# Kernel tuning notes

Hardware: AMD Instinct MI355X
Metric: run time of the kernel (lower is better)

Reference implementation:

```python
import jax, jax.numpy as jnp
import numpy as np

K = 31  # AvgPool2d kernel size
P = 15  # padding


def _box_avg(x):
    """31x31 stride-1 avg pool, count_include_pad=True (PyTorch default):
    separable ones-conv with zero padding, divided by K*K."""
    B, C, H, W = x.shape
    kh = jnp.ones((C, 1, K, 1), x.dtype)
    kw = jnp.ones((C, 1, 1, K), x.dtype)
    dn = ('NCHW', 'OIHW', 'NCHW')
    y = jax.lax.conv_general_dilated(x, kh, (1, 1), [(P, P), (0, 0)],
                                     dimension_numbers=dn, feature_group_count=C)
    y = jax.lax.conv_general_dilated(y, kw, (1, 1), [(0, 0), (P, P)],
                                     dimension_numbers=dn, feature_group_count=C)
    return y / (K * K)


def setup_inputs() -> dict:
    key = jax.random.key(0)
    k1, k2 = jax.random.split(key)
    pred = jax.random.normal(k1, (64, 1, 512, 512), dtype=jnp.float32)
    mask = jax.random.uniform(k2, (64, 1, 512, 512), dtype=jnp.float32)
    return {"pred": pred, "mask": mask}


def reference(pred, mask):
    weit = 1.0 + 5.0 * jnp.abs(_box_avg(mask) - mask)
    p = jax.nn.sigmoid(pred)
    inter = jnp.sum(p * mask * weit, axis=(2, 3))          # [B, C]
    union = jnp.sum((p + mask) * weit, axis=(2, 3))        # [B, C]
    wdiss = 1.0 - (2.0 * inter + 0.5) / (union + 0.5)
    return jnp.mean(wdiss)
```

## Files before the change

### kernel.cpp

```cpp
#include <hip/hip_runtime.h>
#include <math.h>

#define NB 64
#define HH 512
#define WW 512
#define KK 31
#define PP 15
#define TSP 128
#define NSP (HH / TSP)
#define RING 64
#define RMASK (RING - 1)

typedef _Float16 f16;
typedef f16 f16x8 __attribute__((ext_vector_type(8)));
typedef f16 f16x4 __attribute__((ext_vector_type(4)));
typedef f16 f16x2 __attribute__((ext_vector_type(2)));

__device__ __forceinline__ f16x2 shfl_up2(f16x2 v, int delta) {
    int x = __shfl_up(__builtin_bit_cast(int, v), delta);
    return __builtin_bit_cast(f16x2, x);
}
__device__ __forceinline__ f16x2 shfl_dn2(f16x2 v, int delta) {
    int x = __shfl_down(__builtin_bit_cast(int, v), delta);
    return __builtin_bit_cast(f16x2, x);
}
__device__ __forceinline__ f16x2 sel2(bool c, f16x2 v) {
    f16x2 z = {(f16)0, (f16)0};
    return c ? v : z;
}
__device__ __forceinline__ void memfence_sched() { asm volatile("" ::: "memory"); }

__device__ __forceinline__ void load_pair(
        const float* __restrict__ mb, const int y0, const int p,
        const int xbase, float (&va)[8], float (&vb)[8])
{
    const int gy0 = y0 + 2 * p - PP;
    const int gy1 = gy0 + 1;
    if (gy0 >= 0 && gy0 < HH) {
        const float* row = mb + (size_t)gy0 * WW + xbase;
        const float4 u = *(const float4*)(row);
        const float4 v = *(const float4*)(row + 4);
        va[0] = u.x; va[1] = u.y; va[2] = u.z; va[3] = u.w;
        va[4] = v.x; va[5] = v.y; va[6] = v.z; va[7] = v.w;
    } else {
        #pragma unroll
        for (int j = 0; j < 8; ++j) va[j] = 0.0f;
    }
    if (gy1 >= 0 && gy1 < HH) {
        const float* row = mb + (size_t)gy1 * WW + xbase;
        const float4 u = *(const float4*)(row);
        const float4 v = *(const float4*)(row + 4);
        vb[0] = u.x; vb[1] = u.y; vb[2] = u.z; vb[3] = u.w;
        vb[4] = v.x; vb[5] = v.y; vb[6] = v.z; vb[7] = v.w;
    } else {
        #pragma unroll
        for (int j = 0; j < 8; ++j) vb[j] = 0.0f;
    }
}

__device__ __forceinline__ void compute_pair(
        f16 (* __restrict__ Hs)[WW], f16 (* __restrict__ Ms)[WW],
        const int p, const int xbase, const int lane,
        const float (&va)[8], const float (&vb)[8])
{
    const bool lm1 = (lane >= 1);
    const bool lm2 = (lane >= 2);
    const bool lp1 = (lane <= 62);
    const bool lp2 = (lane <= 61);
    const int h0 = 2 * p;

    const int yr0 = h0 - PP;
    if (yr0 >= 0 && yr0 < TSP) {
        f16x8 mv;
        #pragma unroll
        for (int j = 0; j < 8; ++j) mv[j] = (f16)va[j];
        *(f16x8*)&Ms[yr0 & RMASK][xbase] = mv;
    }
    if (yr0 + 1 >= 0 && yr0 + 1 < TSP) {
        f16x8 mv;
        #pragma unroll
        for (int j = 0; j < 8; ++j) mv[j] = (f16)vb[j];
        *(f16x8*)&Ms[(yr0 + 1) & RMASK][xbase] = mv;
    }

    float sa[8], sb[8];
    sa[0] = va[0]; sb[0] = vb[0];
    #pragma unroll
    for (int j = 1; j < 8; ++j) { sa[j] = sa[j-1] + va[j]; sb[j] = sb[j-1] + vb[j]; }

    f16x2 ps[8];
    #pragma unroll
    for (int j = 0; j < 8; ++j)
        ps[j] = __builtin_bit_cast(f16x2, __builtin_amdgcn_cvt_pkrtz(sa[j], sb[j]));
    const f16x2 pT = ps[7];

    f16x2 A[7];
    #pragma unroll
    for (int j = 0; j < 7; ++j) A[j] = shfl_up2(pT - ps[j], 2);
    const f16x2 Bprev = shfl_up2(pT, 1);
    const f16x2 Cfull = shfl_dn2(pT, 1);
    f16x2 Cp[7];
    #pragma unroll
    for (int j = 0; j < 7; ++j) Cp[j] = shfl_dn2(ps[j], 2);

    f16x2 base = pT;
    base += sel2(lm1, Bprev);
    base += sel2(lp1, Cfull);

    f16x8 ha, hb;
    #pragma unroll
    for (int j = 0; j < 8; ++j) {
        f16x2 acc = base;
        if (j < 7) acc += sel2(lm2, A[j]);
        if (j > 0) acc += sel2(lp2, Cp[j-1]);
        ha[j] = acc[0];
        hb[j] = acc[1];
    }
    *(f16x8*)&Hs[h0 & RMASK][xbase] = ha;
    *(f16x8*)&Hs[(h0 + 1) & RMASK][xbase] = hb;
}

__device__ __forceinline__ void phase2_half(
        const float* __restrict__ pb,
        const f16 (* __restrict__ Hs)[WW], const f16 (* __restrict__ Ms)[WW],
        const int y0, const int r0h, const int c,
        float4& I4, float4& U4)
{
    float4 Pq[8];
    #pragma unroll
    for (int i = 0; i < 8; ++i)
        Pq[i] = *(const float4*)(pb + (size_t)(y0 + r0h + i) * WW + c);
    memfence_sched();

    f16x4 hl8[8], he8[8];
    f16x4 accA = {(f16)0, (f16)0, (f16)0, (f16)0};
    f16x4 accB = {(f16)0, (f16)0, (f16)0, (f16)0};
    #pragma unroll
    for (int j = 0; j < 8; ++j) {
        hl8[j] = *(const f16x4*)&Hs[(r0h + j) & RMASK][c];
        accA += hl8[j];
    }
    #pragma unroll
    for (int j = 8; j < 15; ++j) accA += *(const f16x4*)&Hs[(r0h + j) & RMASK][c];
    #pragma unroll
    for (int j = 15; j < 30; ++j) accB += *(const f16x4*)&Hs[(r0h + j) & RMASK][c];
    #pragma unroll
    for (int i = 0; i < 8; ++i) he8[i] = *(const f16x4*)&Hs[(r0h + 30 + i) & RMASK][c];

    float4 B;
    B.x = (float)accA[0] + (float)accB[0];
    B.y = (float)accA[1] + (float)accB[1];
    B.z = (float)accA[2] + (float)accB[2];
    B.w = (float)accA[3] + (float)accB[3];

    const float inv2 = 1.0f / (float)(KK * KK);

    #pragma unroll
    for (int i = 0; i < 8; ++i) {
        const int yr = r0h + i;
        const f16x4 he = he8[i];
        const f16x4 hl = hl8[i];
        const f16x4 mm = *(const f16x4*)&Ms[yr & RMASK][c];
        const float4 p4 = Pq[i];
        const float m0 = (float)mm[0], m1 = (float)mm[1];
        const float m2 = (float)mm[2], m3 = (float)mm[3];

        B.x += (float)he[0]; B.y += (float)he[1]; B.z += (float)he[2]; B.w += (float)he[3];

        const float w0 = fmaf(5.0f, fabsf(fmaf(B.x, inv2, -m0)), 1.0f);
        const float w1 = fmaf(5.0f, fabsf(fmaf(B.y, inv2, -m1)), 1.0f);
        const float w2 = fmaf(5.0f, fabsf(fmaf(B.z, inv2, -m2)), 1.0f);
        const float w3 = fmaf(5.0f, fabsf(fmaf(B.w, inv2, -m3)), 1.0f);
        const float sg0 = __builtin_amdgcn_rcpf(1.0f + __expf(-p4.x));
        const float sg1 = __builtin_amdgcn_rcpf(1.0f + __expf(-p4.y));
        const float sg2 = __builtin_amdgcn_rcpf(1.0f + __expf(-p4.z));
        const float sg3 = __builtin_amdgcn_rcpf(1.0f + __expf(-p4.w));

        I4.x = fmaf(sg0 * m0, w0, I4.x);  U4.x = fmaf(sg0 + m0, w0, U4.x);
        I4.y = fmaf(sg1 * m1, w1, I4.y);  U4.y = fmaf(sg1 + m1, w1, U4.y);
        I4.z = fmaf(sg2 * m2, w2, I4.z);  U4.z = fmaf(sg2 + m2, w2, U4.z);
        I4.w = fmaf(sg3 * m3, w3, I4.w);  U4.w = fmaf(sg3 + m3, w3, U4.w);

        B.x -= (float)hl[0]; B.y -= (float)hl[1]; B.z -= (float)hl[2]; B.w -= (float)hl[3];
    }
}


__global__ __launch_bounds__(512, 2) void dice_fused_kernel(
        const float* __restrict__ pred,
        const float* __restrict__ mask,
        float* __restrict__ part) {
    const int sp = blockIdx.x;
    const int b  = blockIdx.y;
    const int t  = threadIdx.x;
    const int wave = t >> 6;
    const int lane = t & 63;
    const int xbase = lane * 8;

    __shared__ f16 Hs[RING][WW];
    __shared__ f16 Ms[RING][WW];
    __shared__ float red[16];

    const float* mb = mask + (size_t)b * HH * WW;
    const float* pb = pred + (size_t)b * HH * WW;
    const int y0 = sp * TSP;

    #pragma unroll
    for (int k = 0; k < 4; ++k) {
        const int p = k * 8 + wave;
        if (p > 30) continue;
        float va[8], vb[8];
        load_pair(mb, y0, p, xbase, va, vb);
        compute_pair(Hs, Ms, p, xbase, lane, va, vb);
    }
    __syncthreads();

    const int q = t & 127;
    const int g = t >> 7;
    const int c = q * 4;

    float4 I4 = make_float4(0.f, 0.f, 0.f, 0.f);
    float4 U4 = make_float4(0.f, 0.f, 0.f, 0.f);

    float va0[8], vb0[8], va1[8], vb1[8];

    #pragma unroll
    for (int half = 0; half < 4; ++half) {
        const int pf = 31 + 16 * half + wave;
        if (half < 3) {
            load_pair(mb, y0, pf,     xbase, va0, vb0);
            load_pair(mb, y0, pf + 8, xbase, va1, vb1);
            memfence_sched();
        }
        phase2_half(pb, Hs, Ms, y0, 32 * half + g * 8, c, I4, U4);
        __syncthreads();
        if (half < 3) {
            compute_pair(Hs, Ms, pf,     xbase, lane, va0, vb0);
            compute_pair(Hs, Ms, pf + 8, xbase, lane, va1, vb1);
            __syncthreads();
        }
    }

    float inter = I4.x + I4.y + I4.z + I4.w;
    float uni   = U4.x + U4.y + U4.z + U4.w;
    #pragma unroll
    for (int off = 32; off > 0; off >>= 1) {
        inter += __shfl_down(inter, off);
        uni   += __shfl_down(uni, off);
    }
    if (lane == 0) { red[wave] = inter; red[8 + wave] = uni; }
    __syncthreads();
    if (t == 0) {
        float ti = 0.f, tu = 0.f;
        #pragma unroll
        for (int w2 = 0; w2 < 8; ++w2) { ti += red[w2]; tu += red[8 + w2]; }
        const int bid = b * NSP + sp;
        part[bid] = ti;
        part[NB * NSP + bid] = tu;
    }
}

__global__ void dice_final_kernel(const float* __restrict__ part,
                                  float* __restrict__ out) {
    const int t = threadIdx.x;
    float inter = 0.0f, uni = 0.0f;
    #pragma unroll
    for (int s = 0; s < NSP; ++s) {
        inter += part[t * NSP + s];
        uni   += part[NB * NSP + t * NSP + s];
    }
    float wd = 1.0f - (2.0f * inter + 0.5f) / (uni + 0.5f);
    #pragma unroll
    for (int off = 32; off > 0; off >>= 1) wd += __shfl_down(wd, off);
    if (t == 0) out[0] = wd * (1.0f / (float)NB);
}

extern "C" void kernel_launch(void* const* d_in, const int* in_sizes, int n_in,
                              void* d_out, int out_size, void* d_ws, size_t ws_size,
                              hipStream_t stream) {
    const float* pred = (const float*)d_in[0];
    const float* mask = (const float*)d_in[1];
    float* out  = (float*)d_out;
    float* part = (float*)d_ws;

    dim3 grid(NSP, NB);
    dice_fused_kernel<<<grid, 512, 0, stream>>>(pred, mask, part);
    dice_final_kernel<<<1, 64, 0, stream>>>(part, out);
}
```

Before: 146.6 us.

## Split image columns into two halves per block with halo lanes

Each block now handles a 256-column strip, so the grid doubles to 8 blocks per image and shared memory per block is halved. Launch bounds are raised to allow 4 blocks per CU. Wave lanes load a 16-column halo on each side so the horizontal box sum stays exact, while only 32 of 64 lanes store. The register prefetch of the next mask rows, which overlapped with phase 2, is removed, and loads now happen after the barrier. The intent is more blocks and higher occupancy, traded for halo reloads, idle lanes in the horizontal pass, and loss of the load/compute overlap.

```diff
diff --git a/kernel.cpp b/kernel.cpp
--- a/kernel.cpp
+++ b/kernel.cpp
@@ -7,13 +7,13 @@
 #define KK 31
 #define PP 15
 #define TSP 128
-#define NSP (HH / TSP)
+#define CB 256
+#define NSTR 8
 #define RING 64
 #define RMASK (RING - 1)
 
 typedef _Float16 f16;
 typedef f16 f16x8 __attribute__((ext_vector_type(8)));
-typedef f16 f16x4 __attribute__((ext_vector_type(4)));
 typedef f16 f16x2 __attribute__((ext_vector_type(2)));
 
 __device__ __forceinline__ f16x2 shfl_up2(f16x2 v, int delta) {
@@ -24,20 +24,15 @@
     int x = __shfl_down(__builtin_bit_cast(int, v), delta);
     return __builtin_bit_cast(f16x2, x);
 }
-__device__ __forceinline__ f16x2 sel2(bool c, f16x2 v) {
-    f16x2 z = {(f16)0, (f16)0};
-    return c ? v : z;
-}
-__device__ __forceinline__ void memfence_sched() { asm volatile("" ::: "memory"); }
 
 __device__ __forceinline__ void load_pair(
         const float* __restrict__ mb, const int y0, const int p,
-        const int xbase, float (&va)[8], float (&vb)[8])
+        const int xg, const bool lact, float (&va)[8], float (&vb)[8])
 {
     const int gy0 = y0 + 2 * p - PP;
     const int gy1 = gy0 + 1;
-    if (gy0 >= 0 && gy0 < HH) {
-        const float* row = mb + (size_t)gy0 * WW + xbase;
+    if (lact && gy0 >= 0 && gy0 < HH) {
+        const float* row = mb + (size_t)gy0 * WW + xg;
         const float4 u = *(const float4*)(row);
         const float4 v = *(const float4*)(row + 4);
         va[0] = u.x; va[1] = u.y; va[2] = u.z; va[3] = u.w;
@@ -46,8 +41,8 @@
         #pragma unroll
         for (int j = 0; j < 8; ++j) va[j] = 0.0f;
     }
-    if (gy1 >= 0 && gy1 < HH) {
-        const float* row = mb + (size_t)gy1 * WW + xbase;
+    if (lact && gy1 >= 0 && gy1 < HH) {
+        const float* row = mb + (size_t)gy1 * WW + xg;
         const float4 u = *(const float4*)(row);
         const float4 v = *(const float4*)(row + 4);
         vb[0] = u.x; vb[1] = u.y; vb[2] = u.z; vb[3] = u.w;
@@ -59,28 +54,24 @@
 }
 
 __device__ __forceinline__ void compute_pair(
-        f16 (* __restrict__ Hs)[WW], f16 (* __restrict__ Ms)[WW],
-        const int p, const int xbase, const int lane,
+        f16 (* __restrict__ Hs)[CB], f16 (* __restrict__ Ms)[CB],
+        const int p, const int cl, const bool lstore,
         const float (&va)[8], const float (&vb)[8])
 {
-    const bool lm1 = (lane >= 1);
-    const bool lm2 = (lane >= 2);
-    const bool lp1 = (lane <= 62);
-    const bool lp2 = (lane <= 61);
     const int h0 = 2 * p;
 
     const int yr0 = h0 - PP;
-    if (yr0 >= 0 && yr0 < TSP) {
+    if (lstore && yr0 >= 0 && yr0 < TSP) {
         f16x8 mv;
         #pragma unroll
         for (int j = 0; j < 8; ++j) mv[j] = (f16)va[j];
-        *(f16x8*)&Ms[yr0 & RMASK][xbase] = mv;
-    }
-    if (yr0 + 1 >= 0 && yr0 + 1 < TSP) {
+        *(f16x8*)&Ms[yr0 & RMASK][cl] = mv;
+    }
+    if (lstore && yr0 + 1 >= 0 && yr0 + 1 < TSP) {
         f16x8 mv;
         #pragma unroll
         for (int j = 0; j < 8; ++j) mv[j] = (f16)vb[j];
-        *(f16x8*)&Ms[(yr0 + 1) & RMASK][xbase] = mv;
+        *(f16x8*)&Ms[(yr0 + 1) & RMASK][cl] = mv;
     }
 
     float sa[8], sb[8];
@@ -103,146 +94,135 @@
     #pragma unroll
     for (int j = 0; j < 7; ++j) Cp[j] = shfl_dn2(ps[j], 2);
 
-    f16x2 base = pT;
-    base += sel2(lm1, Bprev);
-    base += sel2(lp1, Cfull);
+    const f16x2 base = pT + Bprev + Cfull;
 
     f16x8 ha, hb;
     #pragma unroll
     for (int j = 0; j < 8; ++j) {
         f16x2 acc = base;
-        if (j < 7) acc += sel2(lm2, A[j]);
-        if (j > 0) acc += sel2(lp2, Cp[j-1]);
+        if (j < 7) acc += A[j];
+        if (j > 0) acc += Cp[j-1];
         ha[j] = acc[0];
         hb[j] = acc[1];
     }
-    *(f16x8*)&Hs[h0 & RMASK][xbase] = ha;
-    *(f16x8*)&Hs[(h0 + 1) & RMASK][xbase] = hb;
+    if (lstore) {
+        *(f16x8*)&Hs[h0 & RMASK][cl] = ha;
+        *(f16x8*)&Hs[(h0 + 1) & RMASK][cl] = hb;
+    }
 }
 
 __device__ __forceinline__ void phase2_half(
         const float* __restrict__ pb,
-        const f16 (* __restrict__ Hs)[WW], const f16 (* __restrict__ Ms)[WW],
-        const int y0, const int r0h, const int c,
-        float4& I4, float4& U4)
+        const f16 (* __restrict__ Hs)[CB], const f16 (* __restrict__ Ms)[CB],
+        const int y0, const int r0h, const int cl2, const int cg,
+        float& inter, float& uni)
 {
-    float4 Pq[8];
+    float2 Pq[8];
     #pragma unroll
     for (int i = 0; i < 8; ++i)
-        Pq[i] = *(const float4*)(pb + (size_t)(y0 + r0h + i) * WW + c);
-    memfence_sched();
-
-    f16x4 hl8[8], he8[8];
-    f16x4 accA = {(f16)0, (f16)0, (f16)0, (f16)0};
-    f16x4 accB = {(f16)0, (f16)0, (f16)0, (f16)0};
+        Pq[i] = *(const float2*)(pb + (size_t)(y0 + r0h + i) * WW + cg);
+
+    f16x2 hl8[8], he8[8];
+    f16x2 accA = {(f16)0, (f16)0};
+    f16x2 accB = {(f16)0, (f16)0};
     #pragma unroll
     for (int j = 0; j < 8; ++j) {
-        hl8[j] = *(const f16x4*)&Hs[(r0h + j) & RMASK][c];
+        hl8[j] = *(const f16x2*)&Hs[(r0h + j) & RMASK][cl2];
         accA += hl8[j];
     }
     #pragma unroll
-    for (int j = 8; j < 15; ++j) accA += *(const f16x4*)&Hs[(r0h + j) & RMASK][c];
-    #pragma unroll
-    for (int j = 15; j < 30; ++j) accB += *(const f16x4*)&Hs[(r0h + j) & RMASK][c];
-    #pragma unroll
-    for (int i = 0; i < 8; ++i) he8[i] = *(const f16x4*)&Hs[(r0h + 30 + i) & RMASK][c];
-
-    float4 B;
-    B.x = (float)accA[0] + (float)accB[0];
-    B.y = (float)accA[1] + (float)accB[1];
-    B.z = (float)accA[2] + (float)accB[2];
-    B.w = (float)accA[3] + (float)accB[3];
+    for (int j = 8; j < 15; ++j) accA += *(const f16x2*)&Hs[(r0h + j) & RMASK][cl2];
+    #pragma unroll
+    for (int j = 15; j < 30; ++j) accB += *(const f16x2*)&Hs[(r0h + j) & RMASK][cl2];
+    #pragma unroll
+    for (int i = 0; i < 8; ++i) he8[i] = *(const f16x2*)&Hs[(r0h + 30 + i) & RMASK][cl2];
+
+    float Bx = (float)accA[0] + (float)accB[0];
+    float By = (float)accA[1] + (float)accB[1];
 
     const float inv2 = 1.0f / (float)(KK * KK);
 
     #pragma unroll
     for (int i = 0; i < 8; ++i) {
         const int yr = r0h + i;
-        const f16x4 he = he8[i];
-        const f16x4 hl = hl8[i];
-        const f16x4 mm = *(const f16x4*)&Ms[yr & RMASK][c];
-        const float4 p4 = Pq[i];
+        const f16x2 he = he8[i];
+        const f16x2 hl = hl8[i];
+        const f16x2 mm = *(const f16x2*)&Ms[yr & RMASK][cl2];
+        const float2 p2 = Pq[i];
         const float m0 = (float)mm[0], m1 = (float)mm[1];
-        const float m2 = (float)mm[2], m3 = (float)mm[3];
-
-        B.x += (float)he[0]; B.y += (float)he[1]; B.z += (float)he[2]; B.w += (float)he[3];
-
-        const float w0 = fmaf(5.0f, fabsf(fmaf(B.x, inv2, -m0)), 1.0f);
-        const float w1 = fmaf(5.0f, fabsf(fmaf(B.y, inv2, -m1)), 1.0f);
-        const float w2 = fmaf(5.0f, fabsf(fmaf(B.z, inv2, -m2)), 1.0f);
-        const float w3 = fmaf(5.0f, fabsf(fmaf(B.w, inv2, -m3)), 1.0f);
-        const float sg0 = __builtin_amdgcn_rcpf(1.0f + __expf(-p4.x));
-        const float sg1 = __builtin_amdgcn_rcpf(1.0f + __expf(-p4.y));
-        const float sg2 = __builtin_amdgcn_rcpf(1.0f + __expf(-p4.z));
-        const float sg3 = __builtin_amdgcn_rcpf(1.0f + __expf(-p4.w));
-
-        I4.x = fmaf(sg0 * m0, w0, I4.x);  U4.x = fmaf(sg0 + m0, w0, U4.x);
-        I4.y = fmaf(sg1 * m1, w1, I4.y);  U4.y = fmaf(sg1 + m1, w1, U4.y);
-        I4.z = fmaf(sg2 * m2, w2, I4.z);  U4.z = fmaf(sg2 + m2, w2, U4.z);
-        I4.w = fmaf(sg3 * m3, w3, I4.w);  U4.w = fmaf(sg3 + m3, w3, U4.w);
-
-        B.x -= (float)hl[0]; B.y -= (float)hl[1]; B.z -= (float)hl[2]; B.w -= (float)hl[3];
-    }
-}
-
-
-__global__ __launch_bounds__(512, 2) void dice_fused_kernel(
+
+        Bx += (float)he[0]; By += (float)he[1];
+
+        const float w0 = fmaf(5.0f, fabsf(fmaf(Bx, inv2, -m0)), 1.0f);
+        const float w1 = fmaf(5.0f, fabsf(fmaf(By, inv2, -m1)), 1.0f);
+        const float sg0 = __builtin_amdgcn_rcpf(1.0f + __expf(-p2.x));
+        const float sg1 = __builtin_amdgcn_rcpf(1.0f + __expf(-p2.y));
+
+        inter = fmaf(sg0 * m0, w0, inter);  uni = fmaf(sg0 + m0, w0, uni);
+        inter = fmaf(sg1 * m1, w1, inter);  uni = fmaf(sg1 + m1, w1, uni);
+
+        Bx -= (float)hl[0]; By -= (float)hl[1];
+    }
+}
+
+
+__global__ __launch_bounds__(512, 4) void dice_fused_kernel(
         const float* __restrict__ pred,
         const float* __restrict__ mask,
         float* __restrict__ part) {
-    const int sp = blockIdx.x;
+    const int bi = blockIdx.x;
     const int b  = blockIdx.y;
+    const int sp = bi >> 1;
+    const int c0 = (bi & 1) * CB;
     const int t  = threadIdx.x;
     const int wave = t >> 6;
     const int lane = t & 63;
-    const int xbase = lane * 8;
-
-    __shared__ f16 Hs[RING][WW];
-    __shared__ f16 Ms[RING][WW];
+
+    __shared__ f16 Hs[RING][CB];
+    __shared__ f16 Ms[RING][CB];
     __shared__ float red[16];
 
     const float* mb = mask + (size_t)b * HH * WW;
     const float* pb = pred + (size_t)b * HH * WW;
     const int y0 = sp * TSP;
+
+    const int xg = c0 - 16 + lane * 8;
+    const bool lact   = (lane < 36) && (xg >= 0) && (xg < WW);
+    const bool lstore = (lane >= 2) && (lane <= 33);
+    const int  clp1   = (lane - 2) * 8;
 
     #pragma unroll
     for (int k = 0; k < 4; ++k) {
         const int p = k * 8 + wave;
         if (p > 30) continue;
         float va[8], vb[8];
-        load_pair(mb, y0, p, xbase, va, vb);
-        compute_pair(Hs, Ms, p, xbase, lane, va, vb);
+        load_pair(mb, y0, p, xg, lact, va, vb);
+        compute_pair(Hs, Ms, p, clp1, lstore, va, vb);
     }
     __syncthreads();
 
-    const int q = t & 127;
-    const int g = t >> 7;
-    const int c = q * 4;
-
-    float4 I4 = make_float4(0.f, 0.f, 0.f, 0.f);
-    float4 U4 = make_float4(0.f, 0.f, 0.f, 0.f);
-
-    float va0[8], vb0[8], va1[8], vb1[8];
+    const int q  = t & 127;
+    const int g  = t >> 7;
+    const int cl2 = q * 2;
+    const int cg  = c0 + cl2;
+
+    float inter = 0.0f, uni = 0.0f;
 
     #pragma unroll
     for (int half = 0; half < 4; ++half) {
-        const int pf = 31 + 16 * half + wave;
-        if (half < 3) {
-            load_pair(mb, y0, pf,     xbase, va0, vb0);
-            load_pair(mb, y0, pf + 8, xbase, va1, vb1);
-            memfence_sched();
-        }
-        phase2_half(pb, Hs, Ms, y0, 32 * half + g * 8, c, I4, U4);
+        phase2_half(pb, Hs, Ms, y0, 32 * half + g * 8, cl2, cg, inter, uni);
         __syncthreads();
         if (half < 3) {
-            compute_pair(Hs, Ms, pf,     xbase, lane, va0, vb0);
-            compute_pair(Hs, Ms, pf + 8, xbase, lane, va1, vb1);
+            const int pf = 31 + 16 * half + wave;
+            float va[8], vb[8];
+            load_pair(mb, y0, pf, xg, lact, va, vb);
+            compute_pair(Hs, Ms, pf, clp1, lstore, va, vb);
+            load_pair(mb, y0, pf + 8, xg, lact, va, vb);
+            compute_pair(Hs, Ms, pf + 8, clp1, lstore, va, vb);
             __syncthreads();
         }
     }
 
-    float inter = I4.x + I4.y + I4.z + I4.w;
-    float uni   = U4.x + U4.y + U4.z + U4.w;
     #pragma unroll
     for (int off = 32; off > 0; off >>= 1) {
         inter += __shfl_down(inter, off);
@@ -254,9 +234,9 @@
         float ti = 0.f, tu = 0.f;
         #pragma unroll
         for (int w2 = 0; w2 < 8; ++w2) { ti += red[w2]; tu += red[8 + w2]; }
-        const int bid = b * NSP + sp;
+        const int bid = b * NSTR + bi;
         part[bid] = ti;
-        part[NB * NSP + bid] = tu;
+        part[NB * NSTR + bid] = tu;
     }
 }
 
@@ -265,9 +245,9 @@
     const int t = threadIdx.x;
     float inter = 0.0f, uni = 0.0f;
     #pragma unroll
-    for (int s = 0; s < NSP; ++s) {
-        inter += part[t * NSP + s];
-        uni   += part[NB * NSP + t * NSP + s];
+    for (int s = 0; s < NSTR; ++s) {
+        inter += part[t * NSTR + s];
+        uni   += part[NB * NSTR + t * NSTR + s];
     }
     float wd = 1.0f - (2.0f * inter + 0.5f) / (uni + 0.5f);
     #pragma unroll
@@ -283,7 +263,7 @@
     float* out  = (float*)d_out;
     float* part = (float*)d_ws;
 
-    dim3 grid(NSP, NB);
+    dim3 grid(NSTR, NB);
     dice_fused_kernel<<<grid, 512, 0, stream>>>(pred, mask, part);
     dice_final_kernel<<<1, 64, 0, stream>>>(part, out);
 }
```

After: 145.2 us. About the same (-0.9%).
